# Optimization experiments

Measured on AMD Instinct MI355X. Metric: run time of the kernel, lower is better.

## Reference

```python
import jax, jax.numpy as jnp
import numpy as np
from jax import lax

CONV_SIZE = 5
MORPH_SIZE = 5
TH1_INIT = 0.5
STEP = 0.0005
LO, HI = 0.84, 0.86


def _maxpool(a):
    p = MORPH_SIZE // 2
    return lax.reduce_window(
        a, -jnp.inf, lax.max,
        window_dimensions=(1, 1, MORPH_SIZE, MORPH_SIZE),
        window_strides=(1, 1, 1, 1),
        padding=[(0, 0), (0, 0), (p, p), (p, p)])


def setup_inputs() -> dict:
    key = jax.random.key(0)
    k1, _ = jax.random.split(key)
    x = jax.random.uniform(k1, (8, 4, 1024, 1024), dtype=jnp.float32)
    blur_k = jnp.full((1, 1, CONV_SIZE, CONV_SIZE), 1.0 / CONV_SIZE ** 2, dtype=jnp.float32)
    return {"x": x, "blur_k": blur_k}


def reference(x, blur_k):
    N, c, h, w = x.shape
    xi = x.reshape(N * c, 1, h, w)
    out = lax.conv_general_dilated(
        xi, blur_k, window_strides=(1, 1), padding='SAME',
        dimension_numbers=('NCHW', 'OIHW', 'NCHW')).reshape(N, c, h, w)

    # iterative mean-based threshold (quantile) search, same as the torch while-loops
    out_c = lax.stop_gradient(out)

    def frac_above(th):
        return jnp.mean(jnp.where(out_c > th, 1.0, 0.0))

    th = jnp.float32(TH1_INIT)
    th = lax.while_loop(lambda t: frac_above(t) < LO, lambda t: t - STEP, th)
    th = lax.while_loop(lambda t: frac_above(t) > HI, lambda t: t + STEP, th)

    thr = jnp.where(out > th, 1.0, 0.0)
    # morphological close: max-pool then min-pool (min = -maxpool(-x))
    closed = -_maxpool(-_maxpool(thr))
    return closed  # torch casts to float64; kept float32 (see notes)
```

## Files before the change

kernel.cpp:

```cpp
#include <hip/hip_runtime.h>


#define K_STEPS 1024
#define LO_COUNT 28185723u
#define R_TILE 8
#define PT_ROWS 16

#define OFF_HIST 4096
#define OFF_KQ   16384

__global__ void k_init(const float* __restrict__ bk, unsigned int* __restrict__ U,
                       unsigned int* __restrict__ hist) {
    __shared__ float Tsh[K_STEPS];
    int t = threadIdx.x;
    for (int i = t; i < K_STEPS + 1; i += 256) hist[i] = 0u;
    if (t == 0) {
        float th = 0.5f;
        for (int k = 0; k < K_STEPS; k++) { Tsh[k] = th; th = th - 0.0005f; }
    }
    __syncthreads();
    double c = (double)bk[0] * (1.0 / 8388608.0);
    for (int k = t; k < K_STEPS; k += 256) {
        double T = (double)Tsh[k];
        unsigned int u;
        if (T < 0.0) {
            u = 0u;
        } else {
            u = (unsigned int)(floor(T / c) + 1.0);
            while (u > 0u && (double)(u - 1u) * c > T) u--;
            while (!((double)u * c > T)) u++;
        }
        U[k] = u;
    }
}

__device__ __forceinline__ uint4 cvt4(float4 f) {
    return make_uint4((unsigned int)(f.x * 8388608.0f),
                      (unsigned int)(f.y * 8388608.0f),
                      (unsigned int)(f.z * 8388608.0f),
                      (unsigned int)(f.w * 8388608.0f));
}

__device__ __forceinline__ int find_ki(const unsigned int* __restrict__ Us,
                                       float U0f, unsigned int s) {
    float g = (U0f - (float)s) * 9.5367432e-6f;
    int k = (int)g;
    k = max(0, min(K_STEPS - 1, k));
    while (k > 0 && s >= Us[k - 1]) k--;
    while (k < K_STEPS && s < Us[k]) k++;
    return k;
}

__global__ __launch_bounds__(256) void
k_pass1(const float4* __restrict__ x4, const unsigned int* __restrict__ Ug,
        unsigned int* __restrict__ hist, unsigned short* __restrict__ kq16) {
    __shared__ unsigned int Us[K_STEPS];
    __shared__ unsigned int lh[K_STEPS + 1];
    int tid = threadIdx.x;
    int p = blockIdx.y, y0 = blockIdx.x * R_TILE;
    for (int i = tid; i < K_STEPS; i += 256) Us[i] = Ug[i];
    for (int i = tid; i < K_STEPS + 1; i += 256) lh[i] = 0u;
    __syncthreads();
    float U0f = (float)Us[0];

    const float4* pf = x4 + (size_t)p * 262144;
    int tB = (tid < 255) ? tid + 1 : 0;
    const uint4 z4 = make_uint4(0u, 0u, 0u, 0u);

    uint4 A[4], B[4];
    #pragma unroll
    for (int i = 0; i < 4; i++) {
        int yy = y0 - 2 + i;
        if ((unsigned)yy < 1024u) {
            A[i] = cvt4(pf[yy * 256 + tid]);
            B[i] = cvt4(pf[yy * 256 + tB]);
        } else { A[i] = z4; B[i] = z4; }
    }

    unsigned int cnt0 = 0;
    for (int iy = 0; iy < R_TILE; iy++) {
        int y = y0 + iy, ya = y + 2;
        uint4 An, Bn;
        if ((unsigned)ya < 1024u) {
            An = cvt4(pf[ya * 256 + tid]);
            Bn = cvt4(pf[ya * 256 + tB]);
        } else { An = z4; Bn = z4; }

        unsigned int s0 = A[0].x + A[1].x + A[2].x + A[3].x + An.x;
        unsigned int s1 = A[0].y + A[1].y + A[2].y + A[3].y + An.y;
        unsigned int s2 = A[0].z + A[1].z + A[2].z + A[3].z + An.z;
        unsigned int s3 = A[0].w + A[1].w + A[2].w + A[3].w + An.w;
        unsigned int s4 = B[0].x + B[1].x + B[2].x + B[3].x + Bn.x;
        unsigned int s5 = B[0].y + B[1].y + B[2].y + B[3].y + Bn.y;
        unsigned int s6 = B[0].z + B[1].z + B[2].z + B[3].z + Bn.z;
        unsigned int s7 = B[0].w + B[1].w + B[2].w + B[3].w + Bn.w;

        unsigned int m123 = s1 + s2 + s3;
        unsigned int h45  = s4 + s5;
        unsigned int v0, v1, v2, v3;
        if (tid != 255) {
            v0 = s0 + m123 + s4;
            v1 = m123 + h45;
            v2 = s2 + s3 + h45 + s6;
            v3 = s3 + h45 + s6 + s7;
        } else {
            v0 = s0 + m123;
            v1 = m123;
            v2 = h45 + s6;
            v3 = h45 + s6 + s7;
        }

        int k0 = find_ki(Us, U0f, v0);
        int k1 = find_ki(Us, U0f, v1);
        int k2 = find_ki(Us, U0f, v2);
        int k3 = find_ki(Us, U0f, v3);
        cnt0 += (unsigned)(k0 == 0) + (unsigned)(k1 == 0)
              + (unsigned)(k2 == 0) + (unsigned)(k3 == 0);
        if (k0 > 0) atomicAdd(&lh[k0], 1u);
        if (k1 > 0) atomicAdd(&lh[k1], 1u);
        if (k2 > 0) atomicAdd(&lh[k2], 1u);
        if (k3 > 0) atomicAdd(&lh[k3], 1u);

        unsigned short pa = (unsigned short)(min(k0, 255) | (min(k1, 255) << 8));
        unsigned short pb = (unsigned short)(min(k2, 255) | (min(k3, 255) << 8));
        size_t rb = ((size_t)p * 1024 + (size_t)y) * 512;
        kq16[rb + 2 * tid + 1] = pa;
        kq16[rb + ((tid < 255) ? (2 * tid + 2) : 0)] = pb;

        A[0] = A[1]; A[1] = A[2]; A[2] = A[3]; A[3] = An;
        B[0] = B[1]; B[1] = B[2]; B[2] = B[3]; B[3] = Bn;
    }

    #pragma unroll
    for (int d = 32; d > 0; d >>= 1) cnt0 += __shfl_down(cnt0, d);
    if ((tid & 63) == 0 && cnt0) atomicAdd(&lh[0], cnt0);
    __syncthreads();
    for (int i = tid; i < K_STEPS + 1; i += 256) {
        unsigned int c = lh[i];
        if (c) atomicAdd(&hist[i], c);
    }
}

__global__ __launch_bounds__(256) void
k_post(const unsigned char* __restrict__ kqb, const unsigned int* __restrict__ hist,
       float* __restrict__ out) {
    __shared__ unsigned long long Tt[24 * 16];
    __shared__ unsigned long long Vv[20 * 16];
    __shared__ unsigned long long Dd[20 * 16];
    __shared__ unsigned long long Ww[16 * 16];
    __shared__ unsigned long long Ff[16 * 16];
    __shared__ int ksS;

    int tid = threadIdx.x;
    int p = blockIdx.y, y0 = blockIdx.x * PT_ROWS;

    if (tid < 64) {
        int lane = tid;
        unsigned int h[16], s = 0;
        #pragma unroll
        for (int i = 0; i < 16; i++) { h[i] = hist[lane * 16 + i]; s += h[i]; }
        unsigned int inc = s;
        #pragma unroll
        for (int d = 1; d < 64; d <<= 1) {
            unsigned int t = __shfl_up(inc, d);
            if (lane >= d) inc += t;
        }
        unsigned int excl = inc - s;
        bool cross = (excl < LO_COUNT) && (excl + s >= LO_COUNT);
        unsigned long long m = __ballot(cross);
        if (m) {
            int cl = __ffsll((long long)m) - 1;
            if (lane == cl) {
                unsigned int c = excl; int ks = K_STEPS - 1;
                for (int i = 0; i < 16; i++) { c += h[i]; if (c >= LO_COUNT) { ks = lane * 16 + i; break; } }
                ksS = ks;
            }
        } else if (lane == 0) ksS = K_STEPS - 1;
    }
    __syncthreads();
    int ks = ksS;

    const unsigned char* kp = kqb + (size_t)p * 1048576;
    unsigned short* Tt16 = (unsigned short*)Tt;
    #pragma unroll
    for (int i = 0; i < 6; i++) {
        int ch = tid + 256 * i;
        int r = ch >> 6, cc = ch & 63;
        int pr = y0 - 4 + r;
        unsigned int m = 0u;
        if ((unsigned)pr < 1024u) {
            uint4 q = ((const uint4*)(kp + (size_t)pr * 1024))[cc];
            unsigned int wv;
            wv = q.x;
            m |= (unsigned)((wv & 0xffu) <= (unsigned)ks)
               | ((unsigned)(((wv >> 8) & 0xffu) <= (unsigned)ks) << 1)
               | ((unsigned)(((wv >> 16) & 0xffu) <= (unsigned)ks) << 2)
               | ((unsigned)((wv >> 24) <= (unsigned)ks) << 3);
            wv = q.y;
            m |= ((unsigned)((wv & 0xffu) <= (unsigned)ks) << 4)
               | ((unsigned)(((wv >> 8) & 0xffu) <= (unsigned)ks) << 5)
               | ((unsigned)(((wv >> 16) & 0xffu) <= (unsigned)ks) << 6)
               | ((unsigned)((wv >> 24) <= (unsigned)ks) << 7);
            wv = q.z;
            m |= ((unsigned)((wv & 0xffu) <= (unsigned)ks) << 8)
               | ((unsigned)(((wv >> 8) & 0xffu) <= (unsigned)ks) << 9)
               | ((unsigned)(((wv >> 16) & 0xffu) <= (unsigned)ks) << 10)
               | ((unsigned)((wv >> 24) <= (unsigned)ks) << 11);
            wv = q.w;
            m |= ((unsigned)((wv & 0xffu) <= (unsigned)ks) << 12)
               | ((unsigned)(((wv >> 8) & 0xffu) <= (unsigned)ks) << 13)
               | ((unsigned)(((wv >> 16) & 0xffu) <= (unsigned)ks) << 14)
               | ((unsigned)((wv >> 24) <= (unsigned)ks) << 15);
        }
        Tt16[ch] = (unsigned short)m;
    }
    __syncthreads();

    for (int i = tid; i < 320; i += 256) {
        int vr = i >> 4, wc = i & 15;
        int b = vr * 16 + wc;
        Vv[i] = Tt[b] | Tt[b + 16] | Tt[b + 32] | Tt[b + 48] | Tt[b + 64];
    }
    __syncthreads();

    for (int i = tid; i < 320; i += 256) {
        int vr = i >> 4, wc = i & 15;
        int pr = y0 - 2 + vr;
        if ((unsigned)pr >= 1024u) { Dd[i] = ~0ull; continue; }
        unsigned long long Vc = Vv[i];
        unsigned long long Vl = (wc > 0)  ? Vv[i - 1] : 0ull;
        unsigned long long Vr = (wc < 15) ? Vv[i + 1] : 0ull;
        Dd[i] = Vc
            | (Vc << 1) | (Vl >> 63)
            | (Vc << 2) | (Vl >> 62)
            | (Vc >> 1) | (Vr << 63)
            | (Vc >> 2) | (Vr << 62);
    }
    __syncthreads();

    {
        int wr = tid >> 4, wc = tid & 15;
        int b = wr * 16 + wc;
        Ww[tid] = Dd[b] & Dd[b + 16] & Dd[b + 32] & Dd[b + 48] & Dd[b + 64];
    }
    __syncthreads();

    {
        int wc = tid & 15;
        unsigned long long Wc = Ww[tid];
        unsigned long long Wl = (wc > 0)  ? Ww[tid - 1] : ~0ull;
        unsigned long long Wr = (wc < 15) ? Ww[tid + 1] : ~0ull;
        Ff[tid] = Wc
            & ((Wc << 1) | (Wl >> 63))
            & ((Wc << 2) | (Wl >> 62))
            & ((Wc >> 1) | (Wr << 63))
            & ((Wc >> 2) | (Wr << 62));
    }
    __syncthreads();

    for (int i = 0; i < PT_ROWS; i++) {
        unsigned long long wd = Ff[i * 16 + (tid >> 4)];
        int sh = (tid & 15) * 4;
        float4 f;
        f.x = (float)((wd >> sh) & 1ull);
        f.y = (float)((wd >> (sh + 1)) & 1ull);
        f.z = (float)((wd >> (sh + 2)) & 1ull);
        f.w = (float)((wd >> (sh + 3)) & 1ull);
        ((float4*)(out + (size_t)p * 1048576 + (size_t)(y0 + i) * 1024))[tid] = f;
    }
}

extern "C" void kernel_launch(void* const* d_in, const int* in_sizes, int n_in,
                              void* d_out, int out_size, void* d_ws, size_t ws_size,
                              hipStream_t stream) {
    const float4* x4 = (const float4*)d_in[0];
    const float*  bk = (const float*)d_in[1];
    float* out = (float*)d_out;

    char* ws = (char*)d_ws;
    unsigned int*   Ug   = (unsigned int*)(ws);
    unsigned int*   hist = (unsigned int*)(ws + OFF_HIST);
    unsigned short* kq16 = (unsigned short*)(ws + OFF_KQ);
    const unsigned char* kqb = (const unsigned char*)(ws + OFF_KQ);

    k_init<<<1, 256, 0, stream>>>(bk, Ug, hist);

    dim3 g1(1024 / R_TILE, 32);
    k_pass1<<<g1, 256, 0, stream>>>(x4, Ug, hist, kq16);

    dim3 g2(1024 / PT_ROWS, 32);
    k_post<<<g2, 256, 0, stream>>>(kqb, hist, out);
}
```

Measured before the change: 316.3 us.

## Prefetch next rows, fully unroll tile loop, and use branchless threshold lookup

The row loop is fully unrolled, and the load for the next input row is issued before the current row's sums are computed, so global memory latency overlaps the arithmetic. Boundary rows are clamped and masked instead of branched. The threshold-index search drops its data-dependent while loops in favour of a fixed 4-entry comparison window around the estimated index. Launch bounds now request 4 blocks per CU. This assumes the estimate is always within two steps of the true index, and it may raise register pressure.

```diff
diff --git a/kernel.cpp b/kernel.cpp
--- a/kernel.cpp
+++ b/kernel.cpp
@@ -44,14 +44,13 @@
 __device__ __forceinline__ int find_ki(const unsigned int* __restrict__ Us,
                                        float U0f, unsigned int s) {
     float g = (U0f - (float)s) * 9.5367432e-6f;
-    int k = (int)g;
-    k = max(0, min(K_STEPS - 1, k));
-    while (k > 0 && s >= Us[k - 1]) k--;
-    while (k < K_STEPS && s < Us[k]) k++;
-    return k;
-}
-
-__global__ __launch_bounds__(256) void
+    int lo = (int)g - 2;
+    lo = max(0, min(1019, lo));
+    unsigned int a0 = Us[lo], a1 = Us[lo + 1], a2 = Us[lo + 2], a3 = Us[lo + 3];
+    return lo + (int)(s < a0) + (int)(s < a1) + (int)(s < a2) + (int)(s < a3);
+}
+
+__global__ __launch_bounds__(256, 4) void
 k_pass1(const float4* __restrict__ x4, const unsigned int* __restrict__ Ug,
         unsigned int* __restrict__ hist, unsigned short* __restrict__ kq16) {
     __shared__ unsigned int Us[K_STEPS];
@@ -67,33 +66,38 @@
     int tB = (tid < 255) ? tid + 1 : 0;
     const uint4 z4 = make_uint4(0u, 0u, 0u, 0u);
 
-    uint4 A[4], B[4];
+    uint4 A[5], B[5];
     #pragma unroll
-    for (int i = 0; i < 4; i++) {
+    for (int i = 0; i < 5; i++) {
         int yy = y0 - 2 + i;
-        if ((unsigned)yy < 1024u) {
-            A[i] = cvt4(pf[yy * 256 + tid]);
-            B[i] = cvt4(pf[yy * 256 + tB]);
-        } else { A[i] = z4; B[i] = z4; }
+        int yc = min(max(yy, 0), 1023);
+        float4 fa = pf[yc * 256 + tid];
+        float4 fb = pf[yc * 256 + tB];
+        bool v = (unsigned)yy < 1024u;
+        A[i] = v ? cvt4(fa) : z4;
+        B[i] = v ? cvt4(fb) : z4;
     }
 
     unsigned int cnt0 = 0;
+    #pragma unroll
     for (int iy = 0; iy < R_TILE; iy++) {
-        int y = y0 + iy, ya = y + 2;
-        uint4 An, Bn;
-        if ((unsigned)ya < 1024u) {
-            An = cvt4(pf[ya * 256 + tid]);
-            Bn = cvt4(pf[ya * 256 + tB]);
-        } else { An = z4; Bn = z4; }
-
-        unsigned int s0 = A[0].x + A[1].x + A[2].x + A[3].x + An.x;
-        unsigned int s1 = A[0].y + A[1].y + A[2].y + A[3].y + An.y;
-        unsigned int s2 = A[0].z + A[1].z + A[2].z + A[3].z + An.z;
-        unsigned int s3 = A[0].w + A[1].w + A[2].w + A[3].w + An.w;
-        unsigned int s4 = B[0].x + B[1].x + B[2].x + B[3].x + Bn.x;
-        unsigned int s5 = B[0].y + B[1].y + B[2].y + B[3].y + Bn.y;
-        unsigned int s6 = B[0].z + B[1].z + B[2].z + B[3].z + Bn.z;
-        unsigned int s7 = B[0].w + B[1].w + B[2].w + B[3].w + Bn.w;
+        int y = y0 + iy;
+
+        float4 Na, Nb;
+        if (iy < R_TILE - 1) {
+            int yn = min(y + 3, 1023);
+            Na = pf[yn * 256 + tid];
+            Nb = pf[yn * 256 + tB];
+        }
+
+        unsigned int s0 = A[0].x + A[1].x + A[2].x + A[3].x + A[4].x;
+        unsigned int s1 = A[0].y + A[1].y + A[2].y + A[3].y + A[4].y;
+        unsigned int s2 = A[0].z + A[1].z + A[2].z + A[3].z + A[4].z;
+        unsigned int s3 = A[0].w + A[1].w + A[2].w + A[3].w + A[4].w;
+        unsigned int s4 = B[0].x + B[1].x + B[2].x + B[3].x + B[4].x;
+        unsigned int s5 = B[0].y + B[1].y + B[2].y + B[3].y + B[4].y;
+        unsigned int s6 = B[0].z + B[1].z + B[2].z + B[3].z + B[4].z;
+        unsigned int s7 = B[0].w + B[1].w + B[2].w + B[3].w + B[4].w;
 
         unsigned int m123 = s1 + s2 + s3;
         unsigned int h45  = s4 + s5;
@@ -127,8 +131,13 @@
         kq16[rb + 2 * tid + 1] = pa;
         kq16[rb + ((tid < 255) ? (2 * tid + 2) : 0)] = pb;
 
-        A[0] = A[1]; A[1] = A[2]; A[2] = A[3]; A[3] = An;
-        B[0] = B[1]; B[1] = B[2]; B[2] = B[3]; B[3] = Bn;
+        if (iy < R_TILE - 1) {
+            bool vn = (y + 3) < 1024;
+            A[0] = A[1]; A[1] = A[2]; A[2] = A[3]; A[3] = A[4];
+            A[4] = vn ? cvt4(Na) : z4;
+            B[0] = B[1]; B[1] = B[2]; B[2] = B[3]; B[3] = B[4];
+            B[4] = vn ? cvt4(Nb) : z4;
+        }
     }
 
     #pragma unroll
```

Result: faster. 309.0 us (-2.3%).
